# Kernel tuning notes

Measured on AMD Instinct MI355X. Metric: run time of the kernel, lower is better.

The kernel has to match this reference:

```python
import jax, jax.numpy as jnp
import numpy as np

B, T, D, H = 2, 2048, 1024, 16
DH = D // H
TOPK = 64


def setup_inputs() -> dict:
    key = jax.random.key(0)
    ks = jax.random.split(key, 10)
    s = D ** -0.5
    x = jax.random.normal(ks[0], (B, T, D), dtype=jnp.float32)
    key_padding_mask = jax.random.bernoulli(ks[1], 0.1, (B, T))
    Wq = jax.random.normal(ks[2], (D, D), dtype=jnp.float32) * s
    bq = jnp.zeros((D,), dtype=jnp.float32)
    Wk = jax.random.normal(ks[3], (D, D), dtype=jnp.float32) * s
    bk = jnp.zeros((D,), dtype=jnp.float32)
    Wv = jax.random.normal(ks[4], (D, D), dtype=jnp.float32) * s
    bv = jnp.zeros((D,), dtype=jnp.float32)
    Wo = jax.random.normal(ks[5], (D, D), dtype=jnp.float32) * s
    bo = jnp.zeros((D,), dtype=jnp.float32)
    return {"x": x, "Wq": Wq, "bq": bq, "Wk": Wk, "bk": bk,
            "Wv": Wv, "bv": bv, "Wo": Wo, "bo": bo,
            "key_padding_mask": key_padding_mask, "causal": 1}


def _attention(x, Wq, bq, Wk, bk, Wv, bv, Wo, bo, key_padding_mask, causal):
    b, t, d = x.shape
    dh = d // H

    def heads(y):  # (B,T,D) -> (B,H,T,Dh)
        return y.reshape(b, t, H, dh).transpose(0, 2, 1, 3)

    q = heads(x @ Wq.T + bq)
    k = heads(x @ Wk.T + bk)
    v = heads(x @ Wv.T + bv)

    scale = dh ** -0.5
    logits = jnp.einsum('bhqd,bhkd->bhqk', q, k) * scale  # (B,H,T,T)
    neg = jnp.finfo(logits.dtype).min

    # key padding mask: True blocks key position
    logits = jnp.where(key_padding_mask[:, None, None, :], neg, logits)

    if causal:
        i = jnp.arange(t)[:, None]
        j = jnp.arange(t)[None, :]
        blocked = j > (t - t + i)  # Tq == Tk
        logits = jnp.where(blocked[None, None], neg, logits)

    # hard top-k sparsification: keep top-k logits per row, rest -> -inf
    flat = logits.reshape(-1, t)  # (B*H*T, T)
    vals, idx = jax.lax.top_k(flat, TOPK)
    rows = jnp.arange(flat.shape[0])[:, None]
    sparse = jnp.full_like(flat, neg).at[rows, idx].set(vals)
    sparse = sparse.reshape(logits.shape)

    attn = jax.nn.softmax(sparse, axis=-1)
    out = jnp.einsum('bhqk,bhkd->bhqd', attn, v)  # (B,H,T,Dh)
    out = out.transpose(0, 2, 1, 3).reshape(b, t, d)
    return out @ Wo.T + bo


def reference(x, Wq, bq, Wk, bk, Wv, bv, Wo, bo, key_padding_mask, causal):
    return _attention(x, Wq, bq, Wk, bk, Wv, bv, Wo, bo, key_padding_mask, causal)
```

## Files before the change

### kernel.cpp

```cpp
#include <hip/hip_runtime.h>
#include <hip/hip_bf16.h>
#include <stdint.h>

#define BB 2
#define TT 2048
#define DD 1024
#define NH 16
#define HD 64
#define TOPK 64
#define NEGF (-3.402823466e38f)
#define ORD_NEG 0x00800000u
#define QT 16
#define KT 256
#define SELCAP 96

typedef short short8x __attribute__((ext_vector_type(8)));
typedef float floatx4 __attribute__((ext_vector_type(4)));

__device__ __forceinline__ uint32_t ord_u32(float x) {
    uint32_t b = __float_as_uint(x);
    return (b & 0x80000000u) ? ~b : (b | 0x80000000u);
}
__device__ __forceinline__ float unord(uint32_t u) {
    uint32_t b = (u & 0x80000000u) ? (u ^ 0x80000000u) : ~u;
    return __uint_as_float(b);
}
__device__ __forceinline__ short bf16_rne(float x) {
    uint32_t u = __float_as_uint(x);
    u += 0x7FFFu + ((u >> 16) & 1u);
    return (short)(u >> 16);
}
__device__ __forceinline__ float bf16_to_f(short h) {
    return __uint_as_float(((uint32_t)(uint16_t)h) << 16);
}
__device__ __forceinline__ bool mask_at(const void* m, int mode, int idx) {
    if (mode == 0) return ((const int*)m)[idx] != 0;
    if (mode == 1) return ((const unsigned char*)m)[idx] != 0;
    return ((const float*)m)[idx] != 0.0f;
}

__device__ __forceinline__ uint32_t dpp_wumax(uint32_t v) {
    uint32_t t;
    t = (uint32_t)__builtin_amdgcn_update_dpp(0, (int)v, 0x111, 0xf, 0xf, true); v = v > t ? v : t;
    t = (uint32_t)__builtin_amdgcn_update_dpp(0, (int)v, 0x112, 0xf, 0xf, true); v = v > t ? v : t;
    t = (uint32_t)__builtin_amdgcn_update_dpp(0, (int)v, 0x114, 0xf, 0xf, true); v = v > t ? v : t;
    t = (uint32_t)__builtin_amdgcn_update_dpp(0, (int)v, 0x118, 0xf, 0xf, true); v = v > t ? v : t;
    t = (uint32_t)__builtin_amdgcn_update_dpp(0, (int)v, 0x142, 0xa, 0xf, true); v = v > t ? v : t;
    t = (uint32_t)__builtin_amdgcn_update_dpp(0, (int)v, 0x143, 0xc, 0xf, true); v = v > t ? v : t;
    return (uint32_t)__builtin_amdgcn_readlane((int)v, 63);
}
__device__ __forceinline__ float dpp_fsum(float v) {
    v += __uint_as_float((uint32_t)__builtin_amdgcn_update_dpp(0, (int)__float_as_uint(v), 0x111, 0xf, 0xf, true));
    v += __uint_as_float((uint32_t)__builtin_amdgcn_update_dpp(0, (int)__float_as_uint(v), 0x112, 0xf, 0xf, true));
    v += __uint_as_float((uint32_t)__builtin_amdgcn_update_dpp(0, (int)__float_as_uint(v), 0x114, 0xf, 0xf, true));
    v += __uint_as_float((uint32_t)__builtin_amdgcn_update_dpp(0, (int)__float_as_uint(v), 0x118, 0xf, 0xf, true));
    v += __uint_as_float((uint32_t)__builtin_amdgcn_update_dpp(0, (int)__float_as_uint(v), 0x142, 0xa, 0xf, true));
    v += __uint_as_float((uint32_t)__builtin_amdgcn_update_dpp(0, (int)__float_as_uint(v), 0x143, 0xc, 0xf, true));
    return __uint_as_float((uint32_t)__builtin_amdgcn_readlane((int)__float_as_uint(v), 63));
}

__global__ void __launch_bounds__(1024) build_flags(
    const unsigned char* raw, const int* causalp, int* flags, uint32_t* Mt)
{
    __shared__ int odd_nz, big, s_mode;
    __shared__ uint32_t smt[BB * 64];
    const int tid = threadIdx.x;
    if (tid == 0) { odd_nz = 0; big = 0; }
    if (tid < BB * 64) smt[tid] = 0;
    __syncthreads();
    for (int i = tid; i < BB * TT; i += 1024) {
        unsigned char c = raw[i];
        if ((i & 3) && c) atomicOr(&odd_nz, 1);
        if (c > 1) atomicOr(&big, 1);
    }
    __syncthreads();
    if (tid == 0) {
        int mode = odd_nz ? (big ? 2 : 1) : 0;
        s_mode = mode;
        flags[0] = mode;
        flags[1] = (causalp[0] != 0) ? 1 : 0;
    }
    __syncthreads();
    const int mode = s_mode;
    const int w = tid >> 3, g = tid & 7;
    const int bb = w >> 6, l = w & 63;
    uint32_t bits = 0;
#pragma unroll
    for (int si = 0; si < 4; ++si) {
        int s = g * 4 + si;
        if (mask_at(raw, mode, bb * TT + l + 64 * s)) bits |= (1u << s);
    }
    if (bits) atomicOr(&smt[w], bits);
    __syncthreads();
    if (tid < BB * 64) Mt[tid] = smt[tid];
}

__global__ void __launch_bounds__(256) split_f32(
    const float* __restrict__ in, short* __restrict__ hi, short* __restrict__ lo,
    int n4, float scale)
{
    int i = blockIdx.x * blockDim.x + threadIdx.x;
    if (i >= n4) return;
    float4 v = ((const float4*)in)[i];
    float f[4] = {v.x * scale, v.y * scale, v.z * scale, v.w * scale};
    short hh[4], ll[4];
#pragma unroll
    for (int j = 0; j < 4; ++j) {
        hh[j] = bf16_rne(f[j]);
        ll[j] = bf16_rne(f[j] - bf16_to_f(hh[j]));
    }
    short4 h4; h4.x = hh[0]; h4.y = hh[1]; h4.z = hh[2]; h4.w = hh[3];
    short4 l4; l4.x = ll[0]; l4.y = ll[1]; l4.z = ll[2]; l4.w = ll[3];
    ((short4*)hi)[i] = h4;
    ((short4*)lo)[i] = l4;
}

__global__ void __launch_bounds__(256) split_w4(
    const float* __restrict__ W0, const float* __restrict__ W1,
    const float* __restrict__ W2, const float* __restrict__ W3,
    short* __restrict__ h0, short* __restrict__ l0, short* __restrict__ h1, short* __restrict__ l1,
    short* __restrict__ h2, short* __restrict__ l2, short* __restrict__ h3, short* __restrict__ l3,
    int n4)
{
    int i = blockIdx.x * blockDim.x + threadIdx.x;
    if (i >= n4) return;
    const int w = blockIdx.y;
    const float* in = (w == 0) ? W0 : (w == 1) ? W1 : (w == 2) ? W2 : W3;
    short* hi = (w == 0) ? h0 : (w == 1) ? h1 : (w == 2) ? h2 : h3;
    short* lo = (w == 0) ? l0 : (w == 1) ? l1 : (w == 2) ? l2 : l3;
    float4 v = ((const float4*)in)[i];
    float f[4] = {v.x, v.y, v.z, v.w};
    short hh[4], ll[4];
#pragma unroll
    for (int j = 0; j < 4; ++j) {
        hh[j] = bf16_rne(f[j]);
        ll[j] = bf16_rne(f[j] - bf16_to_f(hh[j]));
    }
    short4 h4; h4.x = hh[0]; h4.y = hh[1]; h4.z = hh[2]; h4.w = hh[3];
    short4 l4; l4.x = ll[0]; l4.y = ll[1]; l4.z = ll[2]; l4.w = ll[3];
    ((short4*)hi)[i] = h4;
    ((short4*)lo)[i] = l4;
}

__global__ void __launch_bounds__(256) gemm_bf16s(
    const short* __restrict__ Ah, const short* __restrict__ Al,
    const short* __restrict__ Bh, const short* __restrict__ Bl,
    const float* __restrict__ bias, float* __restrict__ Cf,
    short* __restrict__ Ch, short* __restrict__ Cl, float scale, int mode, int terms)
{
    const int bid = blockIdx.x;
    const int xcd = bid & 7, slot = bid >> 3;
    const int panel = xcd * 4 + (slot >> 4);
    const int ncol  = slot & 15;
    const int tid = threadIdx.x, lane = tid & 63, wv = tid >> 6;
    const int wr = wv >> 1, wc = wv & 1;
    const int m0 = panel * 128 + wr * 64;
    const int n0 = ncol * 64 + wc * 32;
    const int lrow = lane & 15, lk = (lane >> 4) * 8;

    floatx4 acc[4][2];
#pragma unroll
    for (int i = 0; i < 4; ++i)
#pragma unroll
        for (int j = 0; j < 2; ++j) acc[i][j] = (floatx4){0.f, 0.f, 0.f, 0.f};

    auto ldfr = [&](int kk, short8x* pah, short8x* pal, short8x* pbh, short8x* pbl) {
#pragma unroll
        for (int mb = 0; mb < 4; ++mb) {
            size_t off = (size_t)(m0 + mb * 16 + lrow) * DD + kk + lk;
            pah[mb] = *(const short8x*)(Ah + off);
            if (terms & 1) pal[mb] = *(const short8x*)(Al + off);
        }
#pragma unroll
        for (int nb = 0; nb < 2; ++nb) {
            size_t off = (size_t)(n0 + nb * 16 + lrow) * DD + kk + lk;
            pbh[nb] = *(const short8x*)(Bh + off);
            if (terms & 2) pbl[nb] = *(const short8x*)(Bl + off);
        }
    };
    auto domfma = [&](short8x* pah, short8x* pal, short8x* pbh, short8x* pbl) {
#pragma unroll
        for (int mb = 0; mb < 4; ++mb)
#pragma unroll
            for (int nb = 0; nb < 2; ++nb) {
                acc[mb][nb] = __builtin_amdgcn_mfma_f32_16x16x32_bf16(pah[mb], pbh[nb], acc[mb][nb], 0, 0, 0);
                if (terms & 2)
                    acc[mb][nb] = __builtin_amdgcn_mfma_f32_16x16x32_bf16(pah[mb], pbl[nb], acc[mb][nb], 0, 0, 0);
                if (terms & 1)
                    acc[mb][nb] = __builtin_amdgcn_mfma_f32_16x16x32_bf16(pal[mb], pbh[nb], acc[mb][nb], 0, 0, 0);
            }
    };

    short8x A0[4], L0[4], B0[2], C0[2];
    short8x A1[4], L1[4], B1[2], C1[2];
    ldfr(0, A0, L0, B0, C0);
    for (int kk = 0; kk < DD; kk += 64) {
        ldfr(kk + 32, A1, L1, B1, C1);
        domfma(A0, L0, B0, C0);
        if (kk + 64 < DD) ldfr(kk + 64, A0, L0, B0, C0);
        domfma(A1, L1, B1, C1);
    }

#pragma unroll
    for (int mb = 0; mb < 4; ++mb)
#pragma unroll
        for (int nb = 0; nb < 2; ++nb) {
            int n = n0 + nb * 16 + lrow;
            float bv = bias[n];
#pragma unroll
            for (int j = 0; j < 4; ++j) {
                int m = m0 + mb * 16 + (lane >> 4) * 4 + j;
                float v = acc[mb][nb][j] + bv;
                if (mode == 0) {
                    Cf[(size_t)m * DD + n] = v;
                } else {
                    int b = m >> 11, t = m & (TT - 1), h = n >> 6, dh = n & (HD - 1);
                    size_t idx = (((size_t)b * NH + h) * TT + t) * HD + dh;
                    if (mode == 1) {
                        Cf[idx] = v;
                    } else {
                        v *= scale;
                        short hi16 = bf16_rne(v);
                        Ch[idx] = hi16;
                        Cl[idx] = bf16_rne(v - bf16_to_f(hi16));
                    }
                }
            }
        }
}

__global__ void __launch_bounds__(256) gemm_xwt(
    const float* __restrict__ A, const float* __restrict__ W,
    const float* __restrict__ bias, float* __restrict__ C,
    int M, int N, int K, int split_heads)
{
    __shared__ float As[64][17];
    __shared__ float Ws[64][17];
    const int tid = threadIdx.x;
    const int tx = tid & 15, ty = tid >> 4;
    const int arow = blockIdx.y * 64, bcol = blockIdx.x * 64;
    float acc[4][4] = {};

    for (int k0 = 0; k0 < K; k0 += 16) {
        const int r = tid >> 2, c = (tid & 3) * 4;
        float4 a4 = *(const float4*)(A + (size_t)(arow + r) * K + k0 + c);
        As[r][c] = a4.x; As[r][c + 1] = a4.y; As[r][c + 2] = a4.z; As[r][c + 3] = a4.w;
        float4 w4 = *(const float4*)(W + (size_t)(bcol + r) * K + k0 + c);
        Ws[r][c] = w4.x; Ws[r][c + 1] = w4.y; Ws[r][c + 2] = w4.z; Ws[r][c + 3] = w4.w;
        __syncthreads();
#pragma unroll
        for (int k = 0; k < 16; ++k) {
            float a0 = As[ty * 4 + 0][k], a1 = As[ty * 4 + 1][k];
            float a2 = As[ty * 4 + 2][k], a3 = As[ty * 4 + 3][k];
            float w0 = Ws[tx * 4 + 0][k], w1 = Ws[tx * 4 + 1][k];
            float w2 = Ws[tx * 4 + 2][k], w3 = Ws[tx * 4 + 3][k];
            acc[0][0] += a0 * w0; acc[0][1] += a0 * w1; acc[0][2] += a0 * w2; acc[0][3] += a0 * w3;
            acc[1][0] += a1 * w0; acc[1][1] += a1 * w1; acc[1][2] += a1 * w2; acc[1][3] += a1 * w3;
            acc[2][0] += a2 * w0; acc[2][1] += a2 * w1; acc[2][2] += a2 * w2; acc[2][3] += a2 * w3;
            acc[3][0] += a3 * w0; acc[3][1] += a3 * w1; acc[3][2] += a3 * w2; acc[3][3] += a3 * w3;
        }
        __syncthreads();
    }

#pragma unroll
    for (int i = 0; i < 4; ++i) {
        int m = arow + ty * 4 + i;
#pragma unroll
        for (int j = 0; j < 4; ++j) {
            int n = bcol + tx * 4 + j;
            float v = acc[i][j] + bias[n];
            if (split_heads) {
                int b = m / TT, t = m % TT, h = n / HD, dh = n % HD;
                C[(((size_t)b * NH + h) * TT + t) * HD + dh] = v;
            } else {
                C[(size_t)m * N + n] = v;
            }
        }
    }
}

__global__ void __launch_bounds__(1024) attn_topk(
    const short* __restrict__ Qhi, const short* __restrict__ Qlo,
    const short* __restrict__ Khi, const short* __restrict__ Klo,
    const float* __restrict__ V, const uint32_t* __restrict__ Mt,
    const int* __restrict__ flags, short* __restrict__ Ohi,
    float* __restrict__ Of)
{
    __shared__ float s_S[2][QT][KT + 1];
    __shared__ int2  s_sel[QT][SELCAP];

    const int tid = threadIdx.x, lane = tid & 63, wv = tid >> 6;
    const int d = blockIdx.x;
    const int xcd = d & 7, chunk = d >> 3;
    const int bh = (xcd << 2) | (chunk >> 7);
    const int qt = chunk & 127;
    const int b = bh >> 4, h = bh & 15;
    const int causal = flags[1];
    const size_t hb = (size_t)bh * (size_t)TT * HD;
    const int r0 = qt * QT;
    const int gq = r0 + wv;
    const float* __restrict__ Vh = V + hb;
    const float* __restrict__ Vl = Vh + lane;

    short8x qhi[2], qlo[2];
    {
        const size_t qoff = hb + (size_t)(r0 + (lane & 15)) * HD + (lane >> 4) * 8;
        qhi[0] = *(const short8x*)(Qhi + qoff);
        qhi[1] = *(const short8x*)(Qhi + qoff + 32);
        qlo[0] = *(const short8x*)(Qlo + qoff);
        qlo[1] = *(const short8x*)(Qlo + qoff + 32);
    }

    const uint32_t mwords = Mt[b * 64 + lane];

    uint32_t lgo[32];
#pragma unroll
    for (int i = 0; i < 32; ++i) lgo[i] = ORD_NEG;

    const int lastT = causal ? ((r0 + QT - 1) >> 8) : 7;

#pragma unroll
    for (int t = 0; t < 8; ++t) {
        if (t <= lastT) {
            const size_t koff = hb + (size_t)(t * KT + wv * 16 + (lane & 15)) * HD + (lane >> 4) * 8;
            short8x kh0 = *(const short8x*)(Khi + koff);
            short8x kh1 = *(const short8x*)(Khi + koff + 32);
            short8x kl0 = *(const short8x*)(Klo + koff);
            short8x kl1 = *(const short8x*)(Klo + koff + 32);
            floatx4 acc = {0.f, 0.f, 0.f, 0.f};
            acc = __builtin_amdgcn_mfma_f32_16x16x32_bf16(qhi[0], kh0, acc, 0, 0, 0);
            acc = __builtin_amdgcn_mfma_f32_16x16x32_bf16(qhi[0], kl0, acc, 0, 0, 0);
            acc = __builtin_amdgcn_mfma_f32_16x16x32_bf16(qlo[0], kh0, acc, 0, 0, 0);
            acc = __builtin_amdgcn_mfma_f32_16x16x32_bf16(qhi[1], kh1, acc, 0, 0, 0);
            acc = __builtin_amdgcn_mfma_f32_16x16x32_bf16(qhi[1], kl1, acc, 0, 0, 0);
            acc = __builtin_amdgcn_mfma_f32_16x16x32_bf16(qlo[1], kh1, acc, 0, 0, 0);
#pragma unroll
            for (int j = 0; j < 4; ++j)
                s_S[t & 1][(lane >> 4) * 4 + j][wv * 16 + (lane & 15)] = acc[j];
            __syncthreads();
#pragma unroll
            for (int j = 0; j < 4; ++j) {
                float sv = s_S[t & 1][wv][j * 64 + lane];
                int key = t * KT + j * 64 + lane;
                bool blocked = ((mwords >> (t * 4 + j)) & 1u) || (causal && key > gq);
                lgo[t * 4 + j] = blocked ? ORD_NEG : ord_u32(sv);
            }
        }
    }

    uint32_t moL = 0;
#pragma unroll
    for (int i = 0; i < 32; ++i) {
        uint32_t u = lgo[i];
        moL = u > moL ? u : moL;
    }
    const uint32_t mo = dpp_wumax(moL);

    auto wcount = [&](uint32_t thrv) -> int {
        int c = 0;
#pragma unroll
        for (int i = 0; i < 32; ++i)
            c += (int)__popcll(__ballot(lgo[i] >= thrv));
        return c;
    };

    float outv;
    if (mo == ORD_NEG) {
        float a0 = 0.f, a1 = 0.f, a2 = 0.f, a3 = 0.f;
        for (int j = 0; j < TT; j += 4) {
            a0 += Vh[(j + 0) * HD + lane];
            a1 += Vh[(j + 1) * HD + lane];
            a2 += Vh[(j + 2) * HD + lane];
            a3 += Vh[(j + 3) * HD + lane];
        }
        outv = (a0 + a1 + a2 + a3) * (1.0f / TT);
    } else {
        const float mF = unord(mo);
        uint32_t thr = 0; uint32_t lo_b = 0, hi_b = 0; int done = 0;
        {
            uint32_t p1 = ord_u32(mF - 2.0f);
            int c1 = wcount(p1);
            if (c1 == TOPK) { thr = p1; done = 1; }
            else if (c1 > TOPK) { lo_b = p1; hi_b = mo; }
            else {
                uint32_t p2 = ord_u32(mF - 4.0f);
                int c2 = wcount(p2);
                if (c2 == TOPK) { thr = p2; done = 1; }
                else if (c2 > TOPK) { lo_b = p2; hi_b = p1; }
                else {
                    uint32_t p3 = ord_u32(mF - 15.0f);
                    int c3 = wcount(p3);
                    if (c3 <= TOPK) { thr = p3; done = 1; }
                    else { lo_b = p3; hi_b = p2; }
                }
            }
        }
        if (!done) {
            while (hi_b - lo_b > 1u) {
                uint32_t mid = lo_b + ((hi_b - lo_b) >> 1);
                int c = wcount(mid);
                if (c == TOPK) { lo_b = mid; break; }
                if (c > TOPK) lo_b = mid; else hi_b = mid;
            }
            thr = lo_b;
        }

        float Sp = 0.f;
#pragma unroll
        for (int i = 0; i < 32; ++i) {
            uint32_t u = lgo[i];
            float w = 0.f;
            if (u >= thr) w = __expf(unord(u) - mF);
            Sp += w;
            lgo[i] = (w > 0.f) ? __float_as_uint(w) : 0u;
        }
        const float S = dpp_fsum(Sp);

        int base = 0;
#pragma unroll
        for (int i = 0; i < 32; ++i) {
            uint32_t wbits = lgo[i];
            unsigned long long msk = __ballot(wbits != 0);
            if (wbits) {
                int below = __builtin_amdgcn_mbcnt_hi((uint32_t)(msk >> 32),
                            __builtin_amdgcn_mbcnt_lo((uint32_t)msk, 0));
                int pos = base + below;
                if (pos < SELCAP) {
                    int keyoff = (((i >> 2) * KT + (i & 3) * 64 + lane) << 6);
                    s_sel[wv][pos] = make_int2(keyoff, (int)wbits);
                }
            }
            base += (int)__popcll(msk);
        }
        int cnt = base < SELCAP ? base : SELCAP;

        float acc = 0.f;
        int i2 = 0;
        for (; i2 + 8 <= cnt; i2 += 8) {
            int   kk[8]; float ww[8];
#pragma unroll
            for (int u = 0; u < 8; ++u) {
                int2 e = s_sel[wv][i2 + u];
                kk[u] = __builtin_amdgcn_readfirstlane(e.x);
                ww[u] = __uint_as_float((uint32_t)__builtin_amdgcn_readfirstlane(e.y));
            }
            float pr[8];
#pragma unroll
            for (int u = 0; u < 8; ++u) pr[u] = Vl[kk[u]];
#pragma unroll
            for (int u = 0; u < 8; ++u) acc += ww[u] * pr[u];
        }
        for (; i2 < cnt; ++i2) {
            int2 e = s_sel[wv][i2];
            int k = __builtin_amdgcn_readfirstlane(e.x);
            float w = __uint_as_float((uint32_t)__builtin_amdgcn_readfirstlane(e.y));
            acc += w * Vl[k];
        }
        outv = acc / S;
    }
    const size_t oidx = ((size_t)b * TT + gq) * DD + h * HD + lane;
    if (Of) Of[oidx] = outv;
    else    Ohi[oidx] = bf16_rne(outv);
}

extern "C" void kernel_launch(void* const* d_in, const int* in_sizes, int n_in,
                              void* d_out, int out_size, void* d_ws, size_t ws_size,
                              hipStream_t stream) {
    const float* x  = (const float*)d_in[0];
    const float* Wq = (const float*)d_in[1];
    const float* bq = (const float*)d_in[2];
    const float* Wk = (const float*)d_in[3];
    const float* bk = (const float*)d_in[4];
    const float* Wv = (const float*)d_in[5];
    const float* bv = (const float*)d_in[6];
    const float* Wo = (const float*)d_in[7];
    const float* bo = (const float*)d_in[8];
    const void*  maskp = d_in[9];
    const int*   causalp = (const int*)d_in[10];
    float* out = (float*)d_out;

    char* ws = (char*)d_ws;
    const size_t TEN  = (size_t)BB * TT * DD * sizeof(float);
    const size_t HTEN = TEN / 2;
    const size_t WSZ  = (size_t)DD * DD * 2;
    const size_t NEED = 6 * TEN + 4096;

    const int nx4 = BB * TT * DD / 4, nw4 = DD * DD / 4;

    if (ws_size >= NEED) {
        float* Vf   = (float*)(ws);
        short* xh   = (short*)(ws + TEN);
        short* xl   = (short*)(ws + TEN + HTEN);
        short* Qhi  = (short*)(ws + 2 * TEN);
        short* Qlo  = (short*)(ws + 2 * TEN + HTEN);
        short* Khi  = (short*)(ws + 3 * TEN);
        short* Klo  = (short*)(ws + 3 * TEN + HTEN);
        short* Ohi  = (short*)(ws + 4 * TEN);
        char*  wb   = ws + 5 * TEN;
        short* wqh = (short*)(wb);            short* wql = (short*)(wb + WSZ);
        short* wkh = (short*)(wb + 2 * WSZ);  short* wkl = (short*)(wb + 3 * WSZ);
        short* wvh = (short*)(wb + 4 * WSZ);  short* wvl = (short*)(wb + 5 * WSZ);
        short* woh = (short*)(wb + 6 * WSZ);  short* wol = (short*)(wb + 7 * WSZ);
        int*      flags = (int*)(wb + 8 * WSZ);
        uint32_t* Mt    = (uint32_t*)(wb + 8 * WSZ + 256);

        build_flags<<<1, 1024, 0, stream>>>((const unsigned char*)maskp, causalp, flags, Mt);

        split_f32<<<(nx4 + 255) / 256, 256, 0, stream>>>(x, xh, xl, nx4, 1.0f);
        dim3 wg((nw4 + 255) / 256, 4);
        split_w4<<<wg, 256, 0, stream>>>(Wq, Wk, Wv, Wo,
                                         wqh, wql, wkh, wkl, wvh, wvl, woh, wol, nw4);

        gemm_bf16s<<<512, 256, 0, stream>>>(xh, xl, wqh, wql, bq, nullptr, Qhi, Qlo, 0.125f, 2, 3);
        gemm_bf16s<<<512, 256, 0, stream>>>(xh, xl, wkh, wkl, bk, nullptr, Khi, Klo, 1.0f, 2, 3);
        gemm_bf16s<<<512, 256, 0, stream>>>(xh, xl, wvh, wvl, bv, Vf, nullptr, nullptr, 1.0f, 1, 0);

        attn_topk<<<BB * NH * (TT / QT), 1024, 0, stream>>>(Qhi, Qlo, Khi, Klo, Vf, Mt, flags,
                                                            Ohi, nullptr);

        gemm_bf16s<<<512, 256, 0, stream>>>(Ohi, Ohi, woh, wol, bo, out, nullptr, nullptr, 1.0f, 0, 0);
    } else {
        float* Qf  = (float*)(ws);
        float* Kf  = (float*)(ws + TEN);
        float* Vf  = (float*)(ws + 2 * TEN);
        float* O   = (float*)(ws + 3 * TEN);
        short* Qhi = (short*)(ws + 4 * TEN);
        short* Qlo = (short*)(ws + 4 * TEN + HTEN);
        short* Khi = (short*)(ws + 5 * TEN);
        short* Klo = (short*)(ws + 5 * TEN + HTEN);
        int*      flags = (int*)(ws + 6 * TEN);
        uint32_t* Mt    = (uint32_t*)(ws + 6 * TEN + 256);

        build_flags<<<1, 1024, 0, stream>>>((const unsigned char*)maskp, causalp, flags, Mt);
        dim3 g2(DD / 64, (BB * TT) / 64);
        gemm_xwt<<<g2, 256, 0, stream>>>(x, Wq, bq, Qf, BB * TT, DD, DD, 1);
        gemm_xwt<<<g2, 256, 0, stream>>>(x, Wk, bk, Kf, BB * TT, DD, DD, 1);
        gemm_xwt<<<g2, 256, 0, stream>>>(x, Wv, bv, Vf, BB * TT, DD, DD, 1);
        split_f32<<<(nx4 + 255) / 256, 256, 0, stream>>>(Qf, Qhi, Qlo, nx4, 0.125f);
        split_f32<<<(nx4 + 255) / 256, 256, 0, stream>>>(Kf, Khi, Klo, nx4, 1.0f);
        attn_topk<<<BB * NH * (TT / QT), 1024, 0, stream>>>(Qhi, Qlo, Khi, Klo, Vf, Mt, flags,
                                                            nullptr, O);
        gemm_xwt<<<g2, 256, 0, stream>>>(O, Wo, bo, out, BB * TT, DD, DD, 0);
    }
}
```

Before: 683.1 us.

## Split top-k attention into selection kernel and separate sparse AV gather kernel

Splits the fused attention kernel in two. The first computes logits and the top-k threshold, then writes a packed per-row list of key indices and bf16 weights to global memory. The second, a small-block kernel, gathers V rows and accumulates the weighted sum. The aim is to take the latency-bound V gather out of the 1024-thread selection kernel so each stage gets better occupancy. In exchange it adds a launch and a global round trip, and storing weights in bf16 costs some precision.

```diff
diff --git a/kernel.cpp b/kernel.cpp
--- a/kernel.cpp
+++ b/kernel.cpp
@@ -13,6 +13,7 @@
 #define QT 16
 #define KT 256
 #define SELCAP 96
+#define SENT 0xFFFF0000u
 
 typedef short short8x __attribute__((ext_vector_type(8)));
 typedef float floatx4 __attribute__((ext_vector_type(4)));
@@ -279,15 +280,14 @@
     }
 }
 
-__global__ void __launch_bounds__(1024) attn_topk(
+__global__ void __launch_bounds__(1024) attn_sel(
     const short* __restrict__ Qhi, const short* __restrict__ Qlo,
     const short* __restrict__ Khi, const short* __restrict__ Klo,
     const float* __restrict__ V, const uint32_t* __restrict__ Mt,
-    const int* __restrict__ flags, short* __restrict__ Ohi,
-    float* __restrict__ Of)
+    const int* __restrict__ flags, uint32_t* __restrict__ list,
+    short* __restrict__ Ohi)
 {
     __shared__ float s_S[2][QT][KT + 1];
-    __shared__ int2  s_sel[QT][SELCAP];
 
     const int tid = threadIdx.x, lane = tid & 63, wv = tid >> 6;
     const int d = blockIdx.x;
@@ -300,7 +300,7 @@
     const int r0 = qt * QT;
     const int gq = r0 + wv;
     const float* __restrict__ Vh = V + hb;
-    const float* __restrict__ Vl = Vh + lane;
+    const size_t rowbase = ((size_t)bh * TT + gq) * 64;
 
     short8x qhi[2], qlo[2];
     {
@@ -364,6 +364,187 @@
         return c;
     };
 
+    if (mo == ORD_NEG) {
+        float a0 = 0.f, a1 = 0.f, a2 = 0.f, a3 = 0.f;
+        for (int j = 0; j < TT; j += 4) {
+            a0 += Vh[(j + 0) * HD + lane];
+            a1 += Vh[(j + 1) * HD + lane];
+            a2 += Vh[(j + 2) * HD + lane];
+            a3 += Vh[(j + 3) * HD + lane];
+        }
+        float outv = (a0 + a1 + a2 + a3) * (1.0f / TT);
+        Ohi[((size_t)b * TT + gq) * DD + h * HD + lane] = bf16_rne(outv);
+        list[rowbase + lane] = SENT;
+        return;
+    }
+
+    const float mF = unord(mo);
+    uint32_t thr = 0; uint32_t lo_b = 0, hi_b = 0; int done = 0;
+    {
+        uint32_t p1 = ord_u32(mF - 2.0f);
+        int c1 = wcount(p1);
+        if (c1 == TOPK) { thr = p1; done = 1; }
+        else if (c1 > TOPK) { lo_b = p1; hi_b = mo; }
+        else {
+            uint32_t p2 = ord_u32(mF - 4.0f);
+            int c2 = wcount(p2);
+            if (c2 == TOPK) { thr = p2; done = 1; }
+            else if (c2 > TOPK) { lo_b = p2; hi_b = p1; }
+            else {
+                uint32_t p3 = ord_u32(mF - 15.0f);
+                int c3 = wcount(p3);
+                if (c3 <= TOPK) { thr = p3; done = 1; }
+                else { lo_b = p3; hi_b = p2; }
+            }
+        }
+    }
+    if (!done) {
+        while (hi_b - lo_b > 1u) {
+            uint32_t mid = lo_b + ((hi_b - lo_b) >> 1);
+            int c = wcount(mid);
+            if (c == TOPK) { lo_b = mid; break; }
+            if (c > TOPK) lo_b = mid; else hi_b = mid;
+        }
+        thr = lo_b;
+    }
+
+    int base = 0;
+#pragma unroll
+    for (int i = 0; i < 32; ++i) {
+        uint32_t u = lgo[i];
+        bool sel = (u >= thr);
+        unsigned long long msk = __ballot(sel);
+        if (sel) {
+            int below = __builtin_amdgcn_mbcnt_hi((uint32_t)(msk >> 32),
+                        __builtin_amdgcn_mbcnt_lo((uint32_t)msk, 0));
+            int pos = base + below;
+            if (pos < 64) {
+                float w = __expf(unord(u) - mF);
+                uint32_t key = (uint32_t)((i >> 2) * KT + (i & 3) * 64 + lane);
+                list[rowbase + pos] = (key << 16) | (uint32_t)(uint16_t)bf16_rne(w);
+            }
+        }
+        base += (int)__popcll(msk);
+    }
+    int cnt = base < 64 ? base : 64;
+    for (int p = cnt + lane; p < 64; p += 64) list[rowbase + p] = SENT;
+}
+
+__global__ void __launch_bounds__(256) attn_av(
+    const uint32_t* __restrict__ list, const float* __restrict__ V,
+    short* __restrict__ Ohi)
+{
+    const int lane = threadIdx.x & 63, wv = threadIdx.x >> 6;
+    const int row = blockIdx.x * 4 + wv;
+    const int bh = row >> 11, q = row & (TT - 1);
+    const float* __restrict__ Vl = V + (size_t)bh * TT * HD + lane;
+
+    uint32_t e = list[(size_t)row * 64 + lane];
+    bool valid = (e >> 16) != 0xFFFFu;
+    unsigned long long msk = __ballot(valid);
+    int cnt = (int)__popcll(msk);
+    if (cnt == 0) return;
+
+    float w = valid ? bf16_to_f((short)(e & 0xFFFFu)) : 0.f;
+    const float S = dpp_fsum(w);
+
+    float acc = 0.f;
+    int k = 0;
+    for (; k + 8 <= cnt; k += 8) {
+        int   kk[8]; float ww[8];
+#pragma unroll
+        for (int u = 0; u < 8; ++u) {
+            uint32_t ee = (uint32_t)__builtin_amdgcn_readlane((int)e, k + u);
+            kk[u] = (int)(ee >> 16) * HD;
+            ww[u] = bf16_to_f((short)(ee & 0xFFFFu));
+        }
+        float pr[8];
+#pragma unroll
+        for (int u = 0; u < 8; ++u) pr[u] = Vl[kk[u]];
+#pragma unroll
+        for (int u = 0; u < 8; ++u) acc += ww[u] * pr[u];
+    }
+    for (; k < cnt; ++k) {
+        uint32_t ee = (uint32_t)__builtin_amdgcn_readlane((int)e, k);
+        acc += bf16_to_f((short)(ee & 0xFFFFu)) * Vl[(int)(ee >> 16) * HD];
+    }
+    const int b = bh >> 4, h = bh & 15;
+    Ohi[((size_t)b * TT + q) * DD + h * HD + lane] = bf16_rne(acc / S);
+}
+
+__global__ void __launch_bounds__(1024) attn_full(
+    const short* __restrict__ Qhi, const short* __restrict__ Qlo,
+    const short* __restrict__ Khi, const short* __restrict__ Klo,
+    const float* __restrict__ V, const uint32_t* __restrict__ Mt,
+    const int* __restrict__ flags, float* __restrict__ Of)
+{
+    __shared__ float s_S[2][QT][KT + 1];
+    __shared__ int2  s_sel[QT][SELCAP];
+
+    const int tid = threadIdx.x, lane = tid & 63, wv = tid >> 6;
+    const int d = blockIdx.x;
+    const int xcd = d & 7, chunk = d >> 3;
+    const int bh = (xcd << 2) | (chunk >> 7);
+    const int qt = chunk & 127;
+    const int b = bh >> 4, h = bh & 15;
+    const int causal = flags[1];
+    const size_t hb = (size_t)bh * (size_t)TT * HD;
+    const int r0 = qt * QT;
+    const int gq = r0 + wv;
+    const float* __restrict__ Vh = V + hb;
+    const float* __restrict__ Vl = Vh + lane;
+
+    short8x qhi[2], qlo[2];
+    {
+        const size_t qoff = hb + (size_t)(r0 + (lane & 15)) * HD + (lane >> 4) * 8;
+        qhi[0] = *(const short8x*)(Qhi + qoff);
+        qhi[1] = *(const short8x*)(Qhi + qoff + 32);
+        qlo[0] = *(const short8x*)(Qlo + qoff);
+        qlo[1] = *(const short8x*)(Qlo + qoff + 32);
+    }
+    const uint32_t mwords = Mt[b * 64 + lane];
+    uint32_t lgo[32];
+#pragma unroll
+    for (int i = 0; i < 32; ++i) lgo[i] = ORD_NEG;
+    const int lastT = causal ? ((r0 + QT - 1) >> 8) : 7;
+#pragma unroll
+    for (int t = 0; t < 8; ++t) {
+        if (t <= lastT) {
+            const size_t koff = hb + (size_t)(t * KT + wv * 16 + (lane & 15)) * HD + (lane >> 4) * 8;
+            short8x kh0 = *(const short8x*)(Khi + koff);
+            short8x kh1 = *(const short8x*)(Khi + koff + 32);
+            short8x kl0 = *(const short8x*)(Klo + koff);
+            short8x kl1 = *(const short8x*)(Klo + koff + 32);
+            floatx4 acc = {0.f, 0.f, 0.f, 0.f};
+            acc = __builtin_amdgcn_mfma_f32_16x16x32_bf16(qhi[0], kh0, acc, 0, 0, 0);
+            acc = __builtin_amdgcn_mfma_f32_16x16x32_bf16(qhi[0], kl0, acc, 0, 0, 0);
+            acc = __builtin_amdgcn_mfma_f32_16x16x32_bf16(qlo[0], kh0, acc, 0, 0, 0);
+            acc = __builtin_amdgcn_mfma_f32_16x16x32_bf16(qhi[1], kh1, acc, 0, 0, 0);
+            acc = __builtin_amdgcn_mfma_f32_16x16x32_bf16(qhi[1], kl1, acc, 0, 0, 0);
+            acc = __builtin_amdgcn_mfma_f32_16x16x32_bf16(qlo[1], kh1, acc, 0, 0, 0);
+#pragma unroll
+            for (int j = 0; j < 4; ++j)
+                s_S[t & 1][(lane >> 4) * 4 + j][wv * 16 + (lane & 15)] = acc[j];
+            __syncthreads();
+#pragma unroll
+            for (int j = 0; j < 4; ++j) {
+                float sv = s_S[t & 1][wv][j * 64 + lane];
+                int key = t * KT + j * 64 + lane;
+                bool blocked = ((mwords >> (t * 4 + j)) & 1u) || (causal && key > gq);
+                lgo[t * 4 + j] = blocked ? ORD_NEG : ord_u32(sv);
+            }
+        }
+    }
+    uint32_t moL = 0;
+#pragma unroll
+    for (int i = 0; i < 32; ++i) { uint32_t u = lgo[i]; moL = u > moL ? u : moL; }
+    const uint32_t mo = dpp_wumax(moL);
+    auto wcount = [&](uint32_t thrv) -> int {
+        int c = 0;
+#pragma unroll
+        for (int i = 0; i < 32; ++i) c += (int)__popcll(__ballot(lgo[i] >= thrv));
+        return c;
+    };
     float outv;
     if (mo == ORD_NEG) {
         float a0 = 0.f, a1 = 0.f, a2 = 0.f, a3 = 0.f;
@@ -404,7 +585,6 @@
             }
             thr = lo_b;
         }
-
         float Sp = 0.f;
 #pragma unroll
         for (int i = 0; i < 32; ++i) {
@@ -415,7 +595,6 @@
             lgo[i] = (w > 0.f) ? __float_as_uint(w) : 0u;
         }
         const float S = dpp_fsum(Sp);
-
         int base = 0;
 #pragma unroll
         for (int i = 0; i < 32; ++i) {
@@ -433,24 +612,8 @@
             base += (int)__popcll(msk);
         }
         int cnt = base < SELCAP ? base : SELCAP;
-
         float acc = 0.f;
-        int i2 = 0;
-        for (; i2 + 8 <= cnt; i2 += 8) {
-            int   kk[8]; float ww[8];
-#pragma unroll
-            for (int u = 0; u < 8; ++u) {
-                int2 e = s_sel[wv][i2 + u];
-                kk[u] = __builtin_amdgcn_readfirstlane(e.x);
-                ww[u] = __uint_as_float((uint32_t)__builtin_amdgcn_readfirstlane(e.y));
-            }
-            float pr[8];
-#pragma unroll
-            for (int u = 0; u < 8; ++u) pr[u] = Vl[kk[u]];
-#pragma unroll
-            for (int u = 0; u < 8; ++u) acc += ww[u] * pr[u];
-        }
-        for (; i2 < cnt; ++i2) {
+        for (int i2 = 0; i2 < cnt; ++i2) {
             int2 e = s_sel[wv][i2];
             int k = __builtin_amdgcn_readfirstlane(e.x);
             float w = __uint_as_float((uint32_t)__builtin_amdgcn_readfirstlane(e.y));
@@ -458,9 +621,7 @@
         }
         outv = acc / S;
     }
-    const size_t oidx = ((size_t)b * TT + gq) * DD + h * HD + lane;
-    if (Of) Of[oidx] = outv;
-    else    Ohi[oidx] = bf16_rne(outv);
+    Of[((size_t)b * TT + gq) * DD + h * HD + lane] = outv;
 }
 
 extern "C" void kernel_launch(void* const* d_in, const int* in_sizes, int n_in,
@@ -491,6 +652,7 @@
         float* Vf   = (float*)(ws);
         short* xh   = (short*)(ws + TEN);
         short* xl   = (short*)(ws + TEN + HTEN);
+        uint32_t* list = (uint32_t*)(ws + TEN);
         short* Qhi  = (short*)(ws + 2 * TEN);
         short* Qlo  = (short*)(ws + 2 * TEN + HTEN);
         short* Khi  = (short*)(ws + 3 * TEN);
@@ -515,8 +677,9 @@
         gemm_bf16s<<<512, 256, 0, stream>>>(xh, xl, wkh, wkl, bk, nullptr, Khi, Klo, 1.0f, 2, 3);
         gemm_bf16s<<<512, 256, 0, stream>>>(xh, xl, wvh, wvl, bv, Vf, nullptr, nullptr, 1.0f, 1, 0);
 
-        attn_topk<<<BB * NH * (TT / QT), 1024, 0, stream>>>(Qhi, Qlo, Khi, Klo, Vf, Mt, flags,
-                                                            Ohi, nullptr);
+        attn_sel<<<BB * NH * (TT / QT), 1024, 0, stream>>>(Qhi, Qlo, Khi, Klo, Vf, Mt, flags,
+                                                           list, Ohi);
+        attn_av<<<BB * NH * TT / 4, 256, 0, stream>>>(list, Vf, Ohi);
 
         gemm_bf16s<<<512, 256, 0, stream>>>(Ohi, Ohi, woh, wol, bo, out, nullptr, nullptr, 1.0f, 0, 0);
     } else {
@@ -538,8 +701,7 @@
         gemm_xwt<<<g2, 256, 0, stream>>>(x, Wv, bv, Vf, BB * TT, DD, DD, 1);
         split_f32<<<(nx4 + 255) / 256, 256, 0, stream>>>(Qf, Qhi, Qlo, nx4, 0.125f);
         split_f32<<<(nx4 + 255) / 256, 256, 0, stream>>>(Kf, Khi, Klo, nx4, 1.0f);
-        attn_topk<<<BB * NH * (TT / QT), 1024, 0, stream>>>(Qhi, Qlo, Khi, Klo, Vf, Mt, flags,
-                                                            nullptr, O);
+        attn_full<<<BB * NH * (TT / QT), 1024, 0, stream>>>(Qhi, Qlo, Khi, Klo, Vf, Mt, flags, O);
         gemm_xwt<<<g2, 256, 0, stream>>>(O, Wo, bo, out, BB * TT, DD, DD, 0);
     }
 }
```

Result: no change. 687.3 us (+0.6%).
